# Kernel tuning notes

Measured on AMD Instinct MI355X. Metric: run time of the kernel, lower is better.

The kernel has to match this reference:

```python
import jax, jax.numpy as jnp
import numpy as np

NUM_CLASSES = 10
OUTPUT_DIM = 128
HIDDEN_DIM = 64


def setup_inputs() -> dict:
    key = jax.random.key(0)
    k1, k2, k3, k4, k5, k6 = jax.random.split(key, 6)
    B, S, F = 16, 4096, 512
    X_support = jax.random.normal(k1, (B, S, F), dtype=jnp.float32)
    y_support = jax.random.randint(k2, (B, S), 0, NUM_CLASSES, dtype=jnp.int32)
    # MLP params: Linear(6, HIDDEN) -> GELU -> Linear(HIDDEN, OUTPUT)
    w1 = jax.random.normal(k3, (6, HIDDEN_DIM), dtype=jnp.float32) * (1.0 / np.sqrt(6.0))
    b1 = jax.random.normal(k4, (HIDDEN_DIM,), dtype=jnp.float32) * 0.01
    w2 = jax.random.normal(k5, (HIDDEN_DIM, OUTPUT_DIM), dtype=jnp.float32) * (1.0 / np.sqrt(HIDDEN_DIM))
    b2 = jax.random.normal(k6, (OUTPUT_DIM,), dtype=jnp.float32) * 0.01
    return {"X_support": X_support, "y_support": y_support,
            "w1": w1, "b1": b1, "w2": w2, "b2": b2}


def _feature_target_stats(X, y):
    """Vectorized equivalent of FeatureTargetStatsEncoder per-(batch,feature) loops.
    X: [B, S, F] float, y: [B, S] int class labels. Returns stats [B, F, 6]."""
    B, S, F = X.shape
    missing_rate = jnp.isnan(X).astype(X.dtype).mean(axis=1)           # [B, F]
    Xc = jnp.nan_to_num(X, nan=0.0)
    gmean = Xc.mean(axis=1)                                            # [B, F]
    variance = Xc.var(axis=1)                                          # biased (unbiased=False)
    absX = jnp.abs(Xc)
    mean_abs = absX.mean(axis=1)
    max_abs = absX.max(axis=1)
    # unique_ratio: count distinct values per (b, f) via sort + diff
    xs = jnp.sort(Xc, axis=1)
    n_unique = 1.0 + (jnp.diff(xs, axis=1) != 0).astype(Xc.dtype).sum(axis=1)
    unique_ratio = n_unique / S
    # classification target score: between-class variance / overall variance
    onehot = jax.nn.one_hot(y, NUM_CLASSES, dtype=Xc.dtype)            # [B, S, C]
    counts = onehot.sum(axis=1)                                        # [B, C]
    csum = jnp.einsum('bsc,bsf->bcf', onehot, Xc)                      # [B, C, F]
    cmean = csum / jnp.maximum(counts, 1.0)[:, :, None]
    dev2 = (cmean - gmean[:, None, :]) ** 2
    between = (counts[:, :, None] * dev2).sum(axis=1) / jnp.maximum(counts.sum(axis=1), 1.0)[:, None]
    target_score = between / jnp.maximum(variance, 1e-6)
    stats = jnp.stack([target_score, missing_rate, unique_ratio,
                       variance, mean_abs, max_abs], axis=-1)          # [B, F, 6]
    return jnp.nan_to_num(stats, nan=0.0, posinf=0.0, neginf=0.0)


def reference(X_support, y_support, w1, b1, w2, b2):
    stats = _feature_target_stats(X_support, y_support)                # [B, F, 6]
    h = jax.nn.gelu(stats @ w1 + b1, approximate=False)               # exact GELU like nn.GELU()
    return h @ w2 + b2                                                 # [B, F, OUTPUT_DIM]
```

## Files before the change

### kernel.cpp

```cpp
#include <hip/hip_runtime.h>
#include <math.h>

#define NS 4096
#define NF 512
#define NB 16
#define NC 10
#define HSIZE 8192
#define HMASK 8191
#define HEMPTY 0xFFFFFFFFu
#define TSR 128
#define TSC 16
#define WS_P_OFF  1024
#define WS_XT_OFF (1024 + NB * NF * 16 * 4)

__device__ __forceinline__ float wave_reduce_add(float v) {
    #pragma unroll
    for (int off = 32; off > 0; off >>= 1) v += __shfl_down(v, off, 64);
    return v;
}
__device__ __forceinline__ float wave_reduce_max(float v) {
    #pragma unroll
    for (int off = 32; off > 0; off >>= 1) v = fmaxf(v, __shfl_down(v, off, 64));
    return v;
}

__device__ __forceinline__ unsigned int pat_of(float x) {
    if (x != x) x = 0.f;
    unsigned int p = __float_as_uint(x);
    return (p == 0x80000000u) ? 0u : p;
}

__device__ __forceinline__ float resolve1(unsigned int* hash,
                                          unsigned int s, unsigned int p, unsigned int o) {
    if (o == HEMPTY) return 1.f;
    if (o == p)      return 0.f;
    for (;;) {
        s = (s + 1) & HMASK;
        const unsigned int oo = atomicCAS(&hash[s], HEMPTY, p);
        if (oo == HEMPTY) return 1.f;
        if (oo == p)      return 0.f;
    }
}

__device__ __forceinline__ float hash8(unsigned int* hash, const float4 u, const float4 v) {
    const unsigned int p0 = pat_of(u.x), p1 = pat_of(u.y), p2 = pat_of(u.z), p3 = pat_of(u.w);
    const unsigned int p4 = pat_of(v.x), p5 = pat_of(v.y), p6 = pat_of(v.z), p7 = pat_of(v.w);
    const unsigned int s0 = (p0 * 2654435761u) >> 19, s1 = (p1 * 2654435761u) >> 19;
    const unsigned int s2 = (p2 * 2654435761u) >> 19, s3 = (p3 * 2654435761u) >> 19;
    const unsigned int s4 = (p4 * 2654435761u) >> 19, s5 = (p5 * 2654435761u) >> 19;
    const unsigned int s6 = (p6 * 2654435761u) >> 19, s7 = (p7 * 2654435761u) >> 19;
    const unsigned int o0 = atomicCAS(&hash[s0], HEMPTY, p0);
    const unsigned int o1 = atomicCAS(&hash[s1], HEMPTY, p1);
    const unsigned int o2 = atomicCAS(&hash[s2], HEMPTY, p2);
    const unsigned int o3 = atomicCAS(&hash[s3], HEMPTY, p3);
    const unsigned int o4 = atomicCAS(&hash[s4], HEMPTY, p4);
    const unsigned int o5 = atomicCAS(&hash[s5], HEMPTY, p5);
    const unsigned int o6 = atomicCAS(&hash[s6], HEMPTY, p6);
    const unsigned int o7 = atomicCAS(&hash[s7], HEMPTY, p7);
    float u8 = 0.f;
    u8 += resolve1(hash, s0, p0, o0);
    u8 += resolve1(hash, s1, p1, o1);
    u8 += resolve1(hash, s2, p2, o2);
    u8 += resolve1(hash, s3, p3, o3);
    u8 += resolve1(hash, s4, p4, o4);
    u8 += resolve1(hash, s5, p5, o5);
    u8 += resolve1(hash, s6, p6, o6);
    u8 += resolve1(hash, s7, p7, o7);
    return u8;
}

__launch_bounds__(512, 4)
__global__ void stripe_stats_kernel(const float* __restrict__ X,
                                    float* __restrict__ XT,
                                    const int* __restrict__ y,
                                    float* __restrict__ P,
                                    float* __restrict__ counts) {
    __shared__ float t[TSR][TSC + 1];
    __shared__ int ys[TSR];
    __shared__ int hist[NC];
    const int b   = blockIdx.x;
    const int f0  = blockIdx.y * TSC;
    const int tid = threadIdx.x;
    const bool do_hist = (blockIdx.y == 0);
    if (do_hist && tid < NC) hist[tid] = 0;

    const int lrow = tid >> 2, lq = tid & 3;
    const int col  = tid >> 5, rq = tid & 31;

    const float* Xb = X + (size_t)b * NS * NF + f0 + lq * 4;
    const int*   yb = y + (size_t)b * NS;

    float sum = 0.f, sumsq = 0.f, sumabs = 0.f, maxabs = 0.f, nancnt = 0.f;
    float csum[NC];
    #pragma unroll
    for (int c = 0; c < NC; c++) csum[c] = 0.f;

    float4 xcur = *(const float4*)(Xb + (size_t)lrow * NF);
    int4 ycur = make_int4(0, 0, 0, 0);
    if (tid < TSR / 4) ycur = *(const int4*)(yb + tid * 4);

    for (int it = 0; it < NS / TSR; ++it) {
        const int s0 = it * TSR;
        float4 xnext = xcur; int4 ynext = ycur;
        if (it + 1 < NS / TSR) {
            xnext = *(const float4*)(Xb + (size_t)(s0 + TSR + lrow) * NF);
            if (tid < TSR / 4) ynext = *(const int4*)(yb + s0 + TSR + tid * 4);
        }
        __syncthreads();
        t[lrow][lq * 4 + 0] = xcur.x; t[lrow][lq * 4 + 1] = xcur.y;
        t[lrow][lq * 4 + 2] = xcur.z; t[lrow][lq * 4 + 3] = xcur.w;
        if (tid < TSR / 4) {
            ys[tid * 4 + 0] = ycur.x; ys[tid * 4 + 1] = ycur.y;
            ys[tid * 4 + 2] = ycur.z; ys[tid * 4 + 3] = ycur.w;
        }
        __syncthreads();
        if (do_hist && tid < TSR) atomicAdd(&hist[ys[tid]], 1);

        #pragma unroll
        for (int j = 0; j < 4; j++) {
            const int r = rq + 32 * j;
            float x = t[r][col];
            const int yc = ys[r];
            if (x != x) { nancnt += 1.f; x = 0.f; }
            sum += x;
            sumsq = fmaf(x, x, sumsq);
            const float a = fabsf(x);
            sumabs += a;
            maxabs = fmaxf(maxabs, a);
            #pragma unroll
            for (int c = 0; c < NC; c++) csum[c] += (yc == c) ? x : 0.f;
        }
        float4 wv;
        wv.x = t[rq * 4 + 0][col]; wv.y = t[rq * 4 + 1][col];
        wv.z = t[rq * 4 + 2][col]; wv.w = t[rq * 4 + 3][col];
        *(float4*)(XT + ((size_t)b * NF + f0 + col) * NS + s0 + rq * 4) = wv;

        xcur = xnext; ycur = ynext;
    }

    float st[16] = { sum, sumsq, sumabs, nancnt, maxabs,
                     csum[0], csum[1], csum[2], csum[3], csum[4],
                     csum[5], csum[6], csum[7], csum[8], csum[9], 0.f };
    #pragma unroll
    for (int s = 0; s < 15; s++) {
        float v = st[s];
        #pragma unroll
        for (int off = 16; off > 0; off >>= 1) {
            const float o = __shfl_down(v, off, 32);
            v = (s == 4) ? fmaxf(v, o) : v + o;
        }
        if (rq == 0) P[((size_t)b * NF + f0 + col) * 16 + s] = v;
    }
    if (do_hist) {
        __syncthreads();
        if (tid < NC) counts[b * NC + tid] = (float)hist[tid];
    }
}

__launch_bounds__(512, 8)
__global__ void fused_hash_mlp(const float* __restrict__ XT,
                               const float* __restrict__ P,
                               const float* __restrict__ counts,
                               const float* __restrict__ w1,
                               const float* __restrict__ b1,
                               const float* __restrict__ w2,
                               const float* __restrict__ b2,
                               float* __restrict__ out) {
    __shared__ __align__(16) unsigned int hash[HSIZE];

    const int w = blockIdx.x;
    const int g = (w & 7) * 1024 + (w >> 3);
    const int b = g >> 9;
    const int f = g & (NF - 1);
    const int tid = threadIdx.x;
    const int wave = tid >> 6, lane = tid & 63;

    uint4* h4 = (uint4*)hash;
    const uint4 e4 = make_uint4(HEMPTY, HEMPTY, HEMPTY, HEMPTY);
    #pragma unroll
    for (int i = 0; i < HSIZE / 4 / 512; i++) h4[i * 512 + tid] = e4;
    __syncthreads();

    const float4* Xc4 = (const float4*)(XT + ((size_t)b * NF + f) * NS);
    const float4 xa = Xc4[tid];
    const float4 xb = Xc4[512 + tid];
    float uniq = hash8(hash, xa, xb);

    __syncthreads();

    float* r = (float*)hash;
    float* stats_s = r + 32;
    float* h_s = r + 64;

    uniq = wave_reduce_add(uniq);
    if (lane == 0) r[wave] = uniq;
    __syncthreads();

    if (tid == 0) {
        float u = 0.f;
        #pragma unroll
        for (int i = 0; i < 8; i++) u += r[i];
        const float* Pp = P + ((size_t)b * NF + f) * 16;
        float S[15];
        #pragma unroll
        for (int s = 0; s < 15; s++) S[s] = Pp[s];
        const float invS = 1.f / (float)NS;
        const float gmean    = S[0] * invS;
        const float variance = fmaxf(S[1] * invS - gmean * gmean, 0.f);
        const float mean_abs = S[2] * invS;
        const float missing  = S[3] * invS;
        const float max_abs  = S[4];
        float between = 0.f;
        #pragma unroll
        for (int c = 0; c < NC; c++) {
            const float cnt = counts[b * NC + c];
            const float cm  = S[5 + c] / fmaxf(cnt, 1.f);
            const float d   = cm - gmean;
            between = fmaf(cnt * d, d, between);
        }
        between *= invS;
        const float target = between / fmaxf(variance, 1e-6f);
        float st6[6] = { target, missing, u * invS, variance, mean_abs, max_abs };
        #pragma unroll
        for (int i = 0; i < 6; i++) {
            float v = st6[i];
            if (!(fabsf(v) < INFINITY)) v = 0.f;
            stats_s[i] = v;
        }
    }
    __syncthreads();

    if (tid < 64) {
        float z = b1[tid];
        #pragma unroll
        for (int i = 0; i < 6; i++) z = fmaf(stats_s[i], w1[i * 64 + tid], z);
        h_s[tid] = 0.5f * z * (1.f + erff(z * 0.70710678118654752440f));
    }
    __syncthreads();
    if (tid < 128) {
        float o = b2[tid];
        #pragma unroll
        for (int j = 0; j < 64; j++) o = fmaf(h_s[j], w2[j * 128 + tid], o);
        out[(size_t)g * 128 + tid] = o;
    }
}

__global__ void count_classes_kernel(const int* __restrict__ y, float* __restrict__ counts) {
    __shared__ int hist[NC];
    const int b = blockIdx.x;
    if (threadIdx.x < NC) hist[threadIdx.x] = 0;
    __syncthreads();
    for (int s = threadIdx.x; s < NS; s += blockDim.x)
        atomicAdd(&hist[y[b * NS + s]], 1);
    __syncthreads();
    if (threadIdx.x < NC) counts[b * NC + threadIdx.x] = (float)hist[threadIdx.x];
}

__launch_bounds__(256)
__global__ void fused_stats_mlp_kernel(const float* __restrict__ X,
                                       const int* __restrict__ y,
                                       const float* __restrict__ counts,
                                       const float* __restrict__ w1,
                                       const float* __restrict__ b1,
                                       const float* __restrict__ w2,
                                       const float* __restrict__ b2,
                                       float* __restrict__ out) {
    __shared__ unsigned int hash[HSIZE];
    __shared__ float red[4][16];
    __shared__ float stats_s[6];
    __shared__ float h_s[64];

    const int w = blockIdx.x;
    const int g = (w & 7) * 1024 + (w >> 3);
    const int b = g >> 9;
    const int f = g & (NF - 1);
    const int tid = threadIdx.x;

    #pragma unroll
    for (int i = 0; i < HSIZE / 256; i++) hash[tid + i * 256] = HEMPTY;
    __syncthreads();

    const float* Xp = X + (size_t)b * NS * NF + f;
    const int*   yp = y + b * NS;

    float sum = 0.f, sumsq = 0.f, sumabs = 0.f, maxabs = 0.f, nancnt = 0.f, uniq = 0.f;
    float csum[NC];
    #pragma unroll
    for (int c = 0; c < NC; c++) csum[c] = 0.f;

    #pragma unroll
    for (int k0 = 0; k0 < 16; k0 += 8) {
        float xv[8]; int yv[8];
        #pragma unroll
        for (int k = 0; k < 8; k++) {
            const int s = (k0 + k) * 256 + tid;
            xv[k] = Xp[(size_t)s * NF];
            yv[k] = yp[s];
        }
        #pragma unroll
        for (int k = 0; k < 8; k++) {
            float x = xv[k];
            if (x != x) { nancnt += 1.f; x = 0.f; }
            sum += x;
            sumsq = fmaf(x, x, sumsq);
            const float a = fabsf(x);
            sumabs += a;
            maxabs = fmaxf(maxabs, a);
            const int yc = yv[k];
            #pragma unroll
            for (int c = 0; c < NC; c++) csum[c] += (yc == c) ? x : 0.f;
            unsigned int pat = __float_as_uint(x);
            if (pat == 0x80000000u) pat = 0u;
            unsigned int slot = (pat * 2654435761u) >> 19;
            for (;;) {
                const unsigned int old = atomicCAS(&hash[slot], HEMPTY, pat);
                if (old == HEMPTY) { uniq += 1.f; break; }
                if (old == pat) break;
                slot = (slot + 1) & HMASK;
            }
        }
    }

    sum    = wave_reduce_add(sum);
    sumsq  = wave_reduce_add(sumsq);
    sumabs = wave_reduce_add(sumabs);
    nancnt = wave_reduce_add(nancnt);
    uniq   = wave_reduce_add(uniq);
    maxabs = wave_reduce_max(maxabs);
    #pragma unroll
    for (int c = 0; c < NC; c++) csum[c] = wave_reduce_add(csum[c]);

    const int wave = tid >> 6, lane = tid & 63;
    if (lane == 0) {
        red[wave][0] = sum;    red[wave][1] = sumsq; red[wave][2] = sumabs;
        red[wave][3] = nancnt; red[wave][4] = uniq;  red[wave][5] = maxabs;
        #pragma unroll
        for (int c = 0; c < NC; c++) red[wave][6 + c] = csum[c];
    }
    __syncthreads();

    if (tid == 0) {
        float t[16];
        #pragma unroll
        for (int v = 0; v < 16; v++) t[v] = red[0][v];
        #pragma unroll
        for (int wv = 1; wv < 4; wv++) {
            #pragma unroll
            for (int v = 0; v < 16; v++) {
                if (v == 5) t[v] = fmaxf(t[v], red[wv][v]);
                else        t[v] += red[wv][v];
            }
        }
        const float invS = 1.f / (float)NS;
        const float gmean    = t[0] * invS;
        const float variance = fmaxf(t[1] * invS - gmean * gmean, 0.f);
        const float mean_abs = t[2] * invS;
        const float missing  = t[3] * invS;
        const float n_unique = t[4];
        const float max_abs  = t[5];
        float between = 0.f;
        #pragma unroll
        for (int c = 0; c < NC; c++) {
            const float cnt = counts[b * NC + c];
            const float cm  = t[6 + c] / fmaxf(cnt, 1.f);
            const float d   = cm - gmean;
            between += cnt * d * d;
        }
        between *= invS;
        const float target = between / fmaxf(variance, 1e-6f);
        float st[6] = { target, missing, n_unique * invS, variance, mean_abs, max_abs };
        #pragma unroll
        for (int i = 0; i < 6; i++) {
            float v = st[i];
            if (!(fabsf(v) < INFINITY)) v = 0.f;
            stats_s[i] = v;
        }
    }
    __syncthreads();

    if (tid < 64) {
        float z = b1[tid];
        #pragma unroll
        for (int i = 0; i < 6; i++) z = fmaf(stats_s[i], w1[i * 64 + tid], z);
        h_s[tid] = 0.5f * z * (1.f + erff(z * 0.70710678118654752440f));
    }
    __syncthreads();
    if (tid < 128) {
        float o = b2[tid];
        #pragma unroll
        for (int j = 0; j < 64; j++) o = fmaf(h_s[j], w2[j * 128 + tid], o);
        out[(size_t)g * 128 + tid] = o;
    }
}

extern "C" void kernel_launch(void* const* d_in, const int* in_sizes, int n_in,
                              void* d_out, int out_size, void* d_ws, size_t ws_size,
                              hipStream_t stream) {
    const float* X  = (const float*)d_in[0];
    const int*   y  = (const int*)d_in[1];
    const float* w1 = (const float*)d_in[2];
    const float* b1 = (const float*)d_in[3];
    const float* w2 = (const float*)d_in[4];
    const float* b2 = (const float*)d_in[5];
    float* out    = (float*)d_out;
    float* counts = (float*)d_ws;

    const size_t xt_bytes = (size_t)NB * NF * NS * sizeof(float);
    if (ws_size >= (size_t)WS_XT_OFF + xt_bytes) {
        float* P  = (float*)((char*)d_ws + WS_P_OFF);
        float* XT = (float*)((char*)d_ws + WS_XT_OFF);
        stripe_stats_kernel<<<dim3(NB, NF / TSC), 512, 0, stream>>>(X, XT, y, P, counts);
        fused_hash_mlp<<<NB * NF, 512, 0, stream>>>(XT, P, counts, w1, b1, w2, b2, out);
    } else {
        count_classes_kernel<<<NB, 256, 0, stream>>>(y, counts);
        fused_stats_mlp_kernel<<<NB * NF, 256, 0, stream>>>(X, y, counts, w1, b1, w2, b2, out);
    }
}
```

Measured before the change: 325.8 us.

## Split stripe stats kernel across sequence segments and merge partials downstream

Adds a segment grid dimension so the transpose/stats kernel launches four times as many blocks, each covering a quarter of the sequence. Per-segment partial sums and maxima are written separately and combined in the hash/MLP kernel, and class counts are accumulated with integer atomics after a memset. The XT load in the hash kernel is also issued before the shared hash clear to overlap latency. Costs an extra memset launch and slightly more partial-stat traffic.

```diff
diff --git a/kernel.cpp b/kernel.cpp
--- a/kernel.cpp
+++ b/kernel.cpp
@@ -10,17 +10,15 @@
 #define HEMPTY 0xFFFFFFFFu
 #define TSR 128
 #define TSC 16
+#define NSEG 4
+#define SEGR (NS / NSEG)
 #define WS_P_OFF  1024
-#define WS_XT_OFF (1024 + NB * NF * 16 * 4)
+#define P2_BYTES (NB * NF * NSEG * 16 * 4)
+#define WS_XT_OFF (WS_P_OFF + P2_BYTES)
 
 __device__ __forceinline__ float wave_reduce_add(float v) {
     #pragma unroll
     for (int off = 32; off > 0; off >>= 1) v += __shfl_down(v, off, 64);
-    return v;
-}
-__device__ __forceinline__ float wave_reduce_max(float v) {
-    #pragma unroll
-    for (int off = 32; off > 0; off >>= 1) v = fmaxf(v, __shfl_down(v, off, 64));
     return v;
 }
 
@@ -73,13 +71,14 @@
 __global__ void stripe_stats_kernel(const float* __restrict__ X,
                                     float* __restrict__ XT,
                                     const int* __restrict__ y,
-                                    float* __restrict__ P,
-                                    float* __restrict__ counts) {
+                                    float* __restrict__ P2,
+                                    int* __restrict__ counts_i) {
     __shared__ float t[TSR][TSC + 1];
     __shared__ int ys[TSR];
     __shared__ int hist[NC];
     const int b   = blockIdx.x;
     const int f0  = blockIdx.y * TSC;
+    const int seg = blockIdx.z;
     const int tid = threadIdx.x;
     const bool do_hist = (blockIdx.y == 0);
     if (do_hist && tid < NC) hist[tid] = 0;
@@ -87,6 +86,7 @@
     const int lrow = tid >> 2, lq = tid & 3;
     const int col  = tid >> 5, rq = tid & 31;
 
+    const int sbase = seg * SEGR;
     const float* Xb = X + (size_t)b * NS * NF + f0 + lq * 4;
     const int*   yb = y + (size_t)b * NS;
 
@@ -95,14 +95,14 @@
     #pragma unroll
     for (int c = 0; c < NC; c++) csum[c] = 0.f;
 
-    float4 xcur = *(const float4*)(Xb + (size_t)lrow * NF);
+    float4 xcur = *(const float4*)(Xb + (size_t)(sbase + lrow) * NF);
     int4 ycur = make_int4(0, 0, 0, 0);
-    if (tid < TSR / 4) ycur = *(const int4*)(yb + tid * 4);
-
-    for (int it = 0; it < NS / TSR; ++it) {
-        const int s0 = it * TSR;
+    if (tid < TSR / 4) ycur = *(const int4*)(yb + sbase + tid * 4);
+
+    for (int it = 0; it < SEGR / TSR; ++it) {
+        const int s0 = sbase + it * TSR;
         float4 xnext = xcur; int4 ynext = ycur;
-        if (it + 1 < NS / TSR) {
+        if (it + 1 < SEGR / TSR) {
             xnext = *(const float4*)(Xb + (size_t)(s0 + TSR + lrow) * NF);
             if (tid < TSR / 4) ynext = *(const int4*)(yb + s0 + TSR + tid * 4);
         }
@@ -138,9 +138,9 @@
         xcur = xnext; ycur = ynext;
     }
 
-    float st[16] = { sum, sumsq, sumabs, nancnt, maxabs,
+    float st[15] = { sum, sumsq, sumabs, nancnt, maxabs,
                      csum[0], csum[1], csum[2], csum[3], csum[4],
-                     csum[5], csum[6], csum[7], csum[8], csum[9], 0.f };
+                     csum[5], csum[6], csum[7], csum[8], csum[9] };
     #pragma unroll
     for (int s = 0; s < 15; s++) {
         float v = st[s];
@@ -149,18 +149,19 @@
             const float o = __shfl_down(v, off, 32);
             v = (s == 4) ? fmaxf(v, o) : v + o;
         }
-        if (rq == 0) P[((size_t)b * NF + f0 + col) * 16 + s] = v;
+        if (rq == 0)
+            P2[(((size_t)b * NF + f0 + col) * NSEG + seg) * 16 + s] = v;
     }
     if (do_hist) {
         __syncthreads();
-        if (tid < NC) counts[b * NC + tid] = (float)hist[tid];
+        if (tid < NC) atomicAdd(&counts_i[b * NC + tid], hist[tid]);
     }
 }
 
 __launch_bounds__(512, 8)
 __global__ void fused_hash_mlp(const float* __restrict__ XT,
-                               const float* __restrict__ P,
-                               const float* __restrict__ counts,
+                               const float* __restrict__ P2,
+                               const int* __restrict__ counts_i,
                                const float* __restrict__ w1,
                                const float* __restrict__ b1,
                                const float* __restrict__ w2,
@@ -175,15 +176,16 @@
     const int tid = threadIdx.x;
     const int wave = tid >> 6, lane = tid & 63;
 
-    uint4* h4 = (uint4*)hash;
-    const uint4 e4 = make_uint4(HEMPTY, HEMPTY, HEMPTY, HEMPTY);
-    #pragma unroll
-    for (int i = 0; i < HSIZE / 4 / 512; i++) h4[i * 512 + tid] = e4;
-    __syncthreads();
-
     const float4* Xc4 = (const float4*)(XT + ((size_t)b * NF + f) * NS);
     const float4 xa = Xc4[tid];
     const float4 xb = Xc4[512 + tid];
+
+    uint4* h4 = (uint4*)hash;
+    const uint4 e4 = make_uint4(HEMPTY, HEMPTY, HEMPTY, HEMPTY);
+    #pragma unroll
+    for (int i = 0; i < HSIZE / 4 / 512; i++) h4[i * 512 + tid] = e4;
+    __syncthreads();
+
     float uniq = hash8(hash, xa, xb);
 
     __syncthreads();
@@ -200,10 +202,14 @@
         float u = 0.f;
         #pragma unroll
         for (int i = 0; i < 8; i++) u += r[i];
-        const float* Pp = P + ((size_t)b * NF + f) * 16;
+        const float* Pp = P2 + ((size_t)b * NF + f) * (NSEG * 16);
         float S[15];
         #pragma unroll
-        for (int s = 0; s < 15; s++) S[s] = Pp[s];
+        for (int s = 0; s < 15; s++) {
+            float v0 = Pp[s], v1 = Pp[16 + s], v2 = Pp[32 + s], v3 = Pp[48 + s];
+            S[s] = (s == 4) ? fmaxf(fmaxf(v0, v1), fmaxf(v2, v3))
+                            : (v0 + v1) + (v2 + v3);
+        }
         const float invS = 1.f / (float)NS;
         const float gmean    = S[0] * invS;
         const float variance = fmaxf(S[1] * invS - gmean * gmean, 0.f);
@@ -213,7 +219,7 @@
         float between = 0.f;
         #pragma unroll
         for (int c = 0; c < NC; c++) {
-            const float cnt = counts[b * NC + c];
+            const float cnt = (float)counts_i[b * NC + c];
             const float cm  = S[5 + c] / fmaxf(cnt, 1.f);
             const float d   = cm - gmean;
             between = fmaf(cnt * d, d, between);
@@ -254,6 +260,17 @@
         atomicAdd(&hist[y[b * NS + s]], 1);
     __syncthreads();
     if (threadIdx.x < NC) counts[b * NC + threadIdx.x] = (float)hist[threadIdx.x];
+}
+
+__device__ __forceinline__ float wave_reduce_add64(float v) {
+    #pragma unroll
+    for (int off = 32; off > 0; off >>= 1) v += __shfl_down(v, off, 64);
+    return v;
+}
+__device__ __forceinline__ float wave_reduce_max64(float v) {
+    #pragma unroll
+    for (int off = 32; off > 0; off >>= 1) v = fmaxf(v, __shfl_down(v, off, 64));
+    return v;
 }
 
 __launch_bounds__(256)
@@ -321,14 +338,14 @@
         }
     }
 
-    sum    = wave_reduce_add(sum);
-    sumsq  = wave_reduce_add(sumsq);
-    sumabs = wave_reduce_add(sumabs);
-    nancnt = wave_reduce_add(nancnt);
-    uniq   = wave_reduce_add(uniq);
-    maxabs = wave_reduce_max(maxabs);
-    #pragma unroll
-    for (int c = 0; c < NC; c++) csum[c] = wave_reduce_add(csum[c]);
+    sum    = wave_reduce_add64(sum);
+    sumsq  = wave_reduce_add64(sumsq);
+    sumabs = wave_reduce_add64(sumabs);
+    nancnt = wave_reduce_add64(nancnt);
+    uniq   = wave_reduce_add64(uniq);
+    maxabs = wave_reduce_max64(maxabs);
+    #pragma unroll
+    for (int c = 0; c < NC; c++) csum[c] = wave_reduce_add64(csum[c]);
 
     const int wave = tid >> 6, lane = tid & 63;
     if (lane == 0) {
@@ -402,16 +419,20 @@
     const float* b1 = (const float*)d_in[3];
     const float* w2 = (const float*)d_in[4];
     const float* b2 = (const float*)d_in[5];
-    float* out    = (float*)d_out;
-    float* counts = (float*)d_ws;
+    float* out = (float*)d_out;
 
     const size_t xt_bytes = (size_t)NB * NF * NS * sizeof(float);
     if (ws_size >= (size_t)WS_XT_OFF + xt_bytes) {
-        float* P  = (float*)((char*)d_ws + WS_P_OFF);
+        int*   counts_i = (int*)d_ws;
+        float* P2 = (float*)((char*)d_ws + WS_P_OFF);
         float* XT = (float*)((char*)d_ws + WS_XT_OFF);
-        stripe_stats_kernel<<<dim3(NB, NF / TSC), 512, 0, stream>>>(X, XT, y, P, counts);
-        fused_hash_mlp<<<NB * NF, 512, 0, stream>>>(XT, P, counts, w1, b1, w2, b2, out);
+        hipMemsetAsync(d_ws, 0, NB * NC * sizeof(int), stream);
+        stripe_stats_kernel<<<dim3(NB, NF / TSC, NSEG), 512, 0, stream>>>(
+            X, XT, y, P2, counts_i);
+        fused_hash_mlp<<<NB * NF, 512, 0, stream>>>(
+            XT, P2, counts_i, w1, b1, w2, b2, out);
     } else {
+        float* counts = (float*)d_ws;
         count_classes_kernel<<<NB, 256, 0, stream>>>(y, counts);
         fused_stats_mlp_kernel<<<NB * NF, 256, 0, stream>>>(X, y, counts, w1, b1, w2, b2, out);
     }
```

New measurement: 323.5 us. Within noise of the previous version (-0.7%).
